# Optimization experiments

Measured on AMD Instinct MI355X. Metric: run time of the kernel, lower is better.

The kernel has to match this reference:

```python
import jax, jax.numpy as jnp
import numpy as np

B, S, D_IN, D_MODEL, H = 4, 2048, 1024, 1024, 16
DEPTH = D_MODEL // H  # 64


def setup_inputs() -> dict:
    key = jax.random.key(0)
    ks = jax.random.split(key, 8)
    scale = 1.0 / np.sqrt(D_IN)
    q = jax.random.normal(ks[0], (B, S, D_IN), dtype=jnp.float32)
    k = jax.random.normal(ks[1], (B, S, D_IN), dtype=jnp.float32)
    v = jax.random.normal(ks[2], (B, S, D_IN), dtype=jnp.float32)
    # causal additive mask: 1.0 where attention is disallowed (strictly upper triangle)
    mask = jnp.triu(jnp.ones((S, S), dtype=jnp.float32), k=1)[None, None]
    # parameters stored as [in, out] so projection is x @ W
    wq = jax.random.normal(ks[3], (D_IN, D_MODEL), dtype=jnp.float32) * scale
    wk = jax.random.normal(ks[4], (D_IN, D_MODEL), dtype=jnp.float32) * scale
    wv = jax.random.normal(ks[5], (D_IN, D_MODEL), dtype=jnp.float32) * scale
    wd = jax.random.normal(ks[6], (D_MODEL, D_MODEL), dtype=jnp.float32) * (1.0 / np.sqrt(D_MODEL))
    bd = jax.random.normal(ks[7], (D_MODEL,), dtype=jnp.float32) * 0.01
    return {"q": q, "k": k, "v": v, "mask": mask,
            "wq": wq, "wk": wk, "wv": wv, "wd": wd, "bd": bd}


def _split_heads(x):
    # [B, S, D_MODEL] -> [B, H, S, DEPTH]
    return x.reshape(B, S, H, DEPTH).transpose(0, 2, 1, 3)


def reference(q, k, v, mask, wq, wk, wv, wd, bd):
    qh = _split_heads(q @ wq)
    kh = _split_heads(k @ wk)
    vh = _split_heads(v @ wv)
    logits = jnp.einsum('bhqd,bhkd->bhqk', qh, kh) / np.sqrt(DEPTH)
    logits = logits + mask * (-1e9)
    attn = jax.nn.softmax(logits, axis=-1)  # [B, H, S, S]
    ctx = jnp.einsum('bhqk,bhkd->bhqd', attn, vh)
    concat = ctx.transpose(0, 2, 1, 3).reshape(B, S, D_MODEL)
    out = concat @ wd + bd
    return out, attn
```

## Files before the change

kernel.cpp:

```cpp
#include <hip/hip_runtime.h>
#include <hip/hip_bf16.h>
#include <math.h>

#define B_  4
#define S_  2048
#define DM  1024
#define H_  16

typedef __attribute__((ext_vector_type(8))) short short8;
typedef __attribute__((ext_vector_type(4))) short short4v;
typedef __attribute__((ext_vector_type(4))) float f32x4;

#define BAR_LGKM() do { \
    asm volatile("s_waitcnt lgkmcnt(0)" ::: "memory"); \
    __builtin_amdgcn_s_barrier(); \
    __builtin_amdgcn_sched_barrier(0); \
} while (0)

#define WAVE_FENCE() do { \
    asm volatile("s_waitcnt lgkmcnt(0)" ::: "memory"); \
    __builtin_amdgcn_sched_barrier(0); \
} while (0)

typedef __attribute__((address_space(3))) short      lds_s;
typedef __attribute__((address_space(1))) const short glb_s;
#define GLD16(g, l) __builtin_amdgcn_global_load_lds((glb_s*)(g), (lds_s*)(l), 16, 0, 0)

__device__ __forceinline__ short bf16b(float f) {
    __hip_bfloat16 h = __float2bfloat16(f);
    short s; __builtin_memcpy(&s, &h, 2);
    return s;
}

__device__ __forceinline__ float bf2f(short s) {
    unsigned int u = ((unsigned int)(unsigned short)s) << 16;
    float f; __builtin_memcpy(&f, &u, 4);
    return f;
}

__device__ __forceinline__ short8 cvt8(float4 a, float4 b) {
    short8 o;
    o[0] = bf16b(a.x); o[1] = bf16b(a.y); o[2] = bf16b(a.z); o[3] = bf16b(a.w);
    o[4] = bf16b(b.x); o[5] = bf16b(b.y); o[6] = bf16b(b.z); o[7] = bf16b(b.w);
    return o;
}

__device__ __forceinline__ short8 ldfrag(const short* __restrict__ lds, int row, int c) {
    return *reinterpret_cast<const short8*>(lds + (((row << 3) + (c ^ (row & 7))) << 3));
}

__global__ __launch_bounds__(256)
void tcast(const float* __restrict__ W, short* __restrict__ WT) {
    __shared__ float tile[64][65];
    const int n0 = blockIdx.x << 6, k0 = blockIdx.y << 6;
    const int t = threadIdx.x;
    #pragma unroll
    for (int i = 0; i < 16; ++i) {
        int f = i * 256 + t, r = f >> 6, c = f & 63;
        tile[r][c] = W[(size_t)(k0 + r) * DM + n0 + c];
    }
    __syncthreads();
    #pragma unroll
    for (int i = 0; i < 16; ++i) {
        int f = i * 256 + t, r = f >> 6, c = f & 63;
        WT[(size_t)(n0 + r) * DM + k0 + c] = bf16b(tile[c][r]);
    }
}

template<int EPI, int AF32>
__global__ __launch_bounds__(256)
void gemm_nt(const void* __restrict__ Av, const short* __restrict__ BT,
             const float* __restrict__ bias, short* __restrict__ Cb,
             float* __restrict__ Cf) {
    __shared__ __align__(16) short lA[128 * 64];
    __shared__ __align__(16) short lB[128 * 64];
    const int K = 1024;
    const short* A16 = (const short*)Av;
    const float* A32 = (const float*)Av;
    const int id = blockIdx.x;
    const int swz = ((id & 7) << 6) + (id >> 3);
    const int bm = swz >> 3, bn = swz & 7;
    const int t = threadIdx.x, w = t >> 6, l = t & 63, lg = l >> 4, lr = l & 15;
    const int wm = w >> 1, wn = w & 1;

    const int srow = t >> 1, sw = srow & 7, codd = t & 1;
    const size_t arow = (size_t)(bm * 128 + srow) * K;
    short* la = lA + (srow << 6);

    const int grow = l >> 3;
    const int gcol = ((l & 7) ^ grow) << 3;
    const short* Bg  = BT + (size_t)(bn * 128 + w * 32 + grow) * K + gcol;
    short*       lBw = lB + ((w * 32) << 6);
    const short* Ag  = A16 + (size_t)(bm * 128 + w * 32 + grow) * K + gcol;
    short*       lAw = lA + ((w * 32) << 6);

    f32x4 acc[4][4] = {};
    float4 fa[4][2];
    if (AF32) {
        #pragma unroll
        for (int j = 0; j < 4; ++j) {
            const float* p = A32 + arow + ((codd + (j << 1)) << 3);
            fa[j][0] = *reinterpret_cast<const float4*>(p);
            fa[j][1] = *reinterpret_cast<const float4*>(p + 4);
        }
    }

    for (int k0 = 0; k0 < K; k0 += 64) {
        __syncthreads();
        if (AF32) {
            #pragma unroll
            for (int j = 0; j < 4; ++j) {
                const int c = (codd + (j << 1)) ^ sw;
                *reinterpret_cast<short8*>(la + (c << 3)) = cvt8(fa[j][0], fa[j][1]);
            }
        } else {
            #pragma unroll
            for (int i = 0; i < 4; ++i)
                GLD16(Ag + k0 + (size_t)(i << 3) * K, lAw + (i << 9));
        }
        #pragma unroll
        for (int i = 0; i < 4; ++i)
            GLD16(Bg + k0 + (size_t)(i << 3) * K, lBw + (i << 9));
        __syncthreads();
        if (AF32 && k0 + 64 < K) {
            #pragma unroll
            for (int j = 0; j < 4; ++j) {
                const float* p = A32 + arow + k0 + 64 + ((codd + (j << 1)) << 3);
                fa[j][0] = *reinterpret_cast<const float4*>(p);
                fa[j][1] = *reinterpret_cast<const float4*>(p + 4);
            }
        }
        #pragma unroll
        for (int kk = 0; kk < 2; ++kk) {
            short8 af[4], bfr[4];
            #pragma unroll
            for (int fm = 0; fm < 4; ++fm) af[fm]  = ldfrag(lA, wm * 64 + fm * 16 + lr, kk * 4 + lg);
            #pragma unroll
            for (int fn = 0; fn < 4; ++fn) bfr[fn] = ldfrag(lB, wn * 64 + fn * 16 + lr, kk * 4 + lg);
            #pragma unroll
            for (int fm = 0; fm < 4; ++fm)
                #pragma unroll
                for (int fn = 0; fn < 4; ++fn)
                    acc[fm][fn] = __builtin_amdgcn_mfma_f32_16x16x32_bf16(af[fm], bfr[fn], acc[fm][fn], 0, 0, 0);
        }
    }

    const int rb = bm * 128 + wm * 64 + (lg << 2);
    const int cb = bn * 128 + wn * 64 + lr;
    #pragma unroll
    for (int fm = 0; fm < 4; ++fm) {
        #pragma unroll
        for (int fn = 0; fn < 4; ++fn) {
            const int col = cb + fn * 16;
            if (EPI == 2) {
                const float bv = bias[col];
                #pragma unroll
                for (int r = 0; r < 4; ++r) {
                    const int row = rb + fm * 16 + r;
                    Cf[(size_t)row * DM + col] = acc[fm][fn][r] + bv;
                }
            } else if (EPI == 0) {
                const int h = col >> 6, d = col & 63;
                #pragma unroll
                for (int r = 0; r < 4; ++r) {
                    const int row = rb + fm * 16 + r;
                    const int b = row >> 11, s = row & 2047;
                    Cb[(((size_t)(b * H_ + h) * S_ + s) << 6) + d] = bf16b(acc[fm][fn][r]);
                }
            } else {
                const int h = col >> 6, d = col & 63;
                const int row0 = rb + fm * 16;
                const int b = row0 >> 11, s = row0 & 2047;
                short4v pk;
                #pragma unroll
                for (int r = 0; r < 4; ++r) pk[r] = bf16b(acc[fm][fn][r]);
                *reinterpret_cast<short4v*>(Cb + (((size_t)(b * H_ + h) << 6) + d) * S_ + s) = pk;
            }
        }
    }
}

__global__ __launch_bounds__(512, 4)
void attn_mfma(const short* __restrict__ Qh, const short* __restrict__ Kh,
               const short* __restrict__ VhT, float* __restrict__ attn,
               short* __restrict__ ctxb) {
    __shared__ __align__(16) short smem[128 * 64 + 8 * 16 * 64];
    short* lQ = smem;
    short* lK = smem;
    short* lV = smem + 64 * 64;
    short* lP = smem + 128 * 64;

    const int t = threadIdx.x, w = t >> 6, l = t & 63, lg = l >> 4, lr = l & 15;
    const int n   = (int)blockIdx.x;
    const int xcd = n & 7, rest = n >> 3;
    const int j   = rest & 15, mh = rest >> 4;
    const int bh  = (mh << 3) | xcd;
    const int qt  = 15 - j;
    const int q0  = qt << 7;
    const int h   = bh & 15, b = bh >> 4;
    const float SC = 0.18033688f;

    const short* Qg = Qh  + (((size_t)bh * S_ + q0) << 6);
    const short* Kg = Kh  + ((size_t)bh * S_ << 6);
    const short* Vg = VhT + ((size_t)bh << 6) * S_;

    const int wrow = w * 16;
    const int rloc = q0 + wrow + (lg << 2);
    const int wlast = q0 + wrow + 15;
    const int Kw  = wlast >> 6;
    const int nkb = (q0 + 128) >> 6;

    {
        const int row = t >> 2, c0 = (t & 3) << 1, sw = row & 7;
        const short* src = Qg + ((size_t)row << 6) + (c0 << 3);
        short8 v0 = *reinterpret_cast<const short8*>(src);
        short8 v1 = *reinterpret_cast<const short8*>(src + 8);
        *reinterpret_cast<short8*>(lQ + (((row << 3) + ((c0    ) ^ sw)) << 3)) = v0;
        *reinterpret_cast<short8*>(lQ + (((row << 3) + ((c0 + 1) ^ sw)) << 3)) = v1;
    }
    __syncthreads();

    const short8 aq0 = ldfrag(lQ, wrow + lr, lg);
    const short8 aq1 = ldfrag(lQ, wrow + lr, lg + 4);

    const int srow = t >> 3, sc = t & 7;
    const int sslot = ((srow << 3) + (sc ^ (srow & 7))) << 3;
    const short* Kst = Kg + (srow << 6) + (sc << 3);
    const short* Vst = Vg + (size_t)srow * S_ + (sc << 3);

    float rsum[4] = {0.f, 0.f, 0.f, 0.f};
    short8 vk = *reinterpret_cast<const short8*>(Kst);
    for (int kb = 0; kb < nkb; ++kb) {
        BAR_LGKM();
        *reinterpret_cast<short8*>(lK + sslot) = vk;
        if (kb + 1 < nkb)
            vk = *reinterpret_cast<const short8*>(Kst + ((size_t)(kb + 1) << 12));
        BAR_LGKM();
        if (kb * 64 > wlast) continue;
        f32x4 acc[4] = {};
        #pragma unroll
        for (int t4 = 0; t4 < 4; ++t4) {
            short8 bk0 = ldfrag(lK, t4 * 16 + lr, lg);
            short8 bk1 = ldfrag(lK, t4 * 16 + lr, lg + 4);
            acc[t4] = __builtin_amdgcn_mfma_f32_16x16x32_bf16(aq0, bk0, acc[t4], 0, 0, 0);
            acc[t4] = __builtin_amdgcn_mfma_f32_16x16x32_bf16(aq1, bk1, acc[t4], 0, 0, 0);
        }
        if (kb * 64 + 63 <= q0 + wrow) {
            #pragma unroll
            for (int t4 = 0; t4 < 4; ++t4)
                #pragma unroll
                for (int r = 0; r < 4; ++r)
                    rsum[r] += exp2f(acc[t4][r] * SC);
        } else {
            #pragma unroll
            for (int t4 = 0; t4 < 4; ++t4) {
                const int cabs = kb * 64 + t4 * 16 + lr;
                #pragma unroll
                for (int r = 0; r < 4; ++r)
                    if (cabs <= rloc + r) rsum[r] += exp2f(acc[t4][r] * SC);
            }
        }
    }
    #pragma unroll
    for (int r = 0; r < 4; ++r) {
        #pragma unroll
        for (int m = 1; m < 16; m <<= 1) rsum[r] += __shfl_xor(rsum[r], m);
        rsum[r] = 1.f / rsum[r];
    }

    f32x4 ctxa[4] = {};
    short* lPw = lP + (w << 10);
    short8 vv;
    vk = *reinterpret_cast<const short8*>(Kst);
    vv = *reinterpret_cast<const short8*>(Vst);
    for (int kb = 0; kb < nkb; ++kb) {
        BAR_LGKM();
        *reinterpret_cast<short8*>(lK + sslot) = vk;
        *reinterpret_cast<short8*>(lV + sslot) = vv;
        if (kb + 1 < nkb) {
            vk = *reinterpret_cast<const short8*>(Kst + ((size_t)(kb + 1) << 12));
            vv = *reinterpret_cast<const short8*>(Vst + ((kb + 1) << 6));
        }
        BAR_LGKM();
        if (kb * 64 > wlast) continue;
        f32x4 acc[4] = {};
        #pragma unroll
        for (int t4 = 0; t4 < 4; ++t4) {
            short8 bk0 = ldfrag(lK, t4 * 16 + lr, lg);
            short8 bk1 = ldfrag(lK, t4 * 16 + lr, lg + 4);
            acc[t4] = __builtin_amdgcn_mfma_f32_16x16x32_bf16(aq0, bk0, acc[t4], 0, 0, 0);
            acc[t4] = __builtin_amdgcn_mfma_f32_16x16x32_bf16(aq1, bk1, acc[t4], 0, 0, 0);
        }
        const bool fullt = (kb * 64 + 63 <= q0 + wrow);
        #pragma unroll
        for (int t4 = 0; t4 < 4; ++t4) {
            const int cl = t4 * 16 + lr;
            const int cabs = kb * 64 + cl;
            #pragma unroll
            for (int r = 0; r < 4; ++r) {
                float p;
                if (!fullt && cabs > rloc + r) p = 0.f;
                else p = exp2f(acc[t4][r] * SC) * rsum[r];
                const int prow = (lg << 2) + r;
                lPw[(prow << 6) + (((t4 * 2 + (lr >> 3)) ^ (prow & 7)) << 3) + (l & 7)] = bf16b(p);
            }
        }
        WAVE_FENCE();
        {
            float* abase = attn + ((size_t)bh * S_ + q0 + wrow) * S_ + kb * 64;
            const int colc = (l & 15) << 2;
            const int ch0  = (l & 15) >> 1;
            const int half = ((l & 15) & 1) << 2;
            #pragma unroll
            for (int rr = 0; rr < 4; ++rr) {
                const int row = (l >> 4) + (rr << 2);
                short4v p4 = *reinterpret_cast<const short4v*>(
                    lPw + (row << 6) + ((ch0 ^ (row & 7)) << 3) + half);
                f32x4 pv = {bf2f(p4[0]), bf2f(p4[1]), bf2f(p4[2]), bf2f(p4[3])};
                *reinterpret_cast<f32x4*>(abase + (size_t)row * S_ + colc) = pv;
            }
        }
        short8 pa0 = ldfrag(lPw, lr, lg);
        short8 pa1 = ldfrag(lPw, lr, lg + 4);
        #pragma unroll
        for (int td = 0; td < 4; ++td) {
            short8 v0 = ldfrag(lV, td * 16 + lr, lg);
            short8 v1 = ldfrag(lV, td * 16 + lr, lg + 4);
            ctxa[td] = __builtin_amdgcn_mfma_f32_16x16x32_bf16(pa0, v0, ctxa[td], 0, 0, 0);
            ctxa[td] = __builtin_amdgcn_mfma_f32_16x16x32_bf16(pa1, v1, ctxa[td], 0, 0, 0);
        }
    }

    short* cbase = ctxb + ((size_t)(b * S_) + q0 + wrow + (lg << 2)) * DM + (h << 6);
    #pragma unroll
    for (int td = 0; td < 4; ++td)
        #pragma unroll
        for (int r = 0; r < 4; ++r)
            cbase[(size_t)r * DM + td * 16 + lr] = bf16b(ctxa[td][r]);

    {
        const f32x4 z = {0.f, 0.f, 0.f, 0.f};
        const int zs = (Kw + 1) << 6;
        const int colc = (l & 15) << 2;
        #pragma unroll
        for (int rr = 0; rr < 4; ++rr) {
            const int row = q0 + wrow + (l >> 4) + (rr << 2);
            float* rowp = attn + ((size_t)bh * S_ + row) * S_;
            for (int c = zs + colc; c < S_; c += 64)
                *reinterpret_cast<f32x4*>(rowp + c) = z;
        }
    }
}

extern "C" void kernel_launch(void* const* d_in, const int* in_sizes, int n_in,
                              void* d_out, int out_size, void* d_ws, size_t ws_size,
                              hipStream_t stream) {
    const float* q  = (const float*)d_in[0];
    const float* k  = (const float*)d_in[1];
    const float* v  = (const float*)d_in[2];
    const float* wq = (const float*)d_in[4];
    const float* wk = (const float*)d_in[5];
    const float* wv = (const float*)d_in[6];
    const float* wd = (const float*)d_in[7];
    const float* bd = (const float*)d_in[8];

    float* out  = (float*)d_out;
    float* attn = (float*)d_out + (size_t)B_ * S_ * DM;

    char* wsc = (char*)d_ws;
    short* ctxb = (short*)wsc;
    short* wT0 = (short*)(wsc + ((size_t)16 << 20));
    short* wT1 = (short*)(wsc + ((size_t)18 << 20));
    short* wT2 = (short*)(wsc + ((size_t)20 << 20));
    short* wT3 = (short*)(wsc + ((size_t)22 << 20));
    short* Qh  = (short*)(wsc + ((size_t)24 << 20));
    short* Kh  = (short*)(wsc + ((size_t)40 << 20));
    short* VhT = (short*)(wsc + ((size_t)56 << 20));

    const dim3 b256(256);
    hipLaunchKernelGGL(tcast, dim3(16, 16), b256, 0, stream, wq, wT0);
    hipLaunchKernelGGL(tcast, dim3(16, 16), b256, 0, stream, wk, wT1);
    hipLaunchKernelGGL(tcast, dim3(16, 16), b256, 0, stream, wv, wT2);
    hipLaunchKernelGGL(tcast, dim3(16, 16), b256, 0, stream, wd, wT3);

    hipLaunchKernelGGL((gemm_nt<0, 1>), dim3(512), b256, 0, stream, q, wT0, nullptr, Qh,  nullptr);
    hipLaunchKernelGGL((gemm_nt<0, 1>), dim3(512), b256, 0, stream, k, wT1, nullptr, Kh,  nullptr);
    hipLaunchKernelGGL((gemm_nt<1, 1>), dim3(512), b256, 0, stream, v, wT2, nullptr, VhT, nullptr);

    hipLaunchKernelGGL(attn_mfma, dim3(1024), dim3(512), 0, stream,
                       Qh, Kh, VhT, attn, ctxb);

    hipLaunchKernelGGL((gemm_nt<2, 0>), dim3(512), b256, 0, stream, ctxb, wT3, bd, nullptr, out);
}
```

Baseline: 450.2 us.

## Shrink attention query tile to 64 rows with 256-thread blocks

Result: no change. 441.6 us (-1.9%).

```diff
diff --git a/kernel.cpp b/kernel.cpp
--- a/kernel.cpp
+++ b/kernel.cpp
@@ -180,23 +180,23 @@
     }
 }
 
-__global__ __launch_bounds__(512, 4)
+__global__ __launch_bounds__(256, 4)
 void attn_mfma(const short* __restrict__ Qh, const short* __restrict__ Kh,
                const short* __restrict__ VhT, float* __restrict__ attn,
                short* __restrict__ ctxb) {
-    __shared__ __align__(16) short smem[128 * 64 + 8 * 16 * 64];
+    __shared__ __align__(16) short smem[64 * 64 * 2 + 4 * 16 * 64];
     short* lQ = smem;
     short* lK = smem;
     short* lV = smem + 64 * 64;
-    short* lP = smem + 128 * 64;
+    short* lP = smem + 64 * 64 * 2;
 
     const int t = threadIdx.x, w = t >> 6, l = t & 63, lg = l >> 4, lr = l & 15;
     const int n   = (int)blockIdx.x;
     const int xcd = n & 7, rest = n >> 3;
-    const int j   = rest & 15, mh = rest >> 4;
+    const int j   = rest & 31, mh = rest >> 5;
     const int bh  = (mh << 3) | xcd;
-    const int qt  = 15 - j;
-    const int q0  = qt << 7;
+    const int qt  = 31 - j;
+    const int q0  = qt << 6;
     const int h   = bh & 15, b = bh >> 4;
     const float SC = 0.18033688f;
 
@@ -206,37 +206,38 @@
 
     const int wrow = w * 16;
     const int rloc = q0 + wrow + (lg << 2);
-    const int wlast = q0 + wrow + 15;
-    const int Kw  = wlast >> 6;
-    const int nkb = (q0 + 128) >> 6;
+    const int nkb = qt + 1;
+
+    const int srow = t >> 2, sc0 = (t & 3) << 1, ssw = srow & 7;
+    const int sslot0 = ((srow << 3) + ((sc0    ) ^ ssw)) << 3;
+    const int sslot1 = ((srow << 3) + ((sc0 + 1) ^ ssw)) << 3;
+    const short* Kst = Kg + (srow << 6) + (sc0 << 3);
+    const short* Vst = Vg + (size_t)srow * S_ + (sc0 << 3);
 
     {
-        const int row = t >> 2, c0 = (t & 3) << 1, sw = row & 7;
-        const short* src = Qg + ((size_t)row << 6) + (c0 << 3);
+        const short* src = Qg + (srow << 6) + (sc0 << 3);
         short8 v0 = *reinterpret_cast<const short8*>(src);
         short8 v1 = *reinterpret_cast<const short8*>(src + 8);
-        *reinterpret_cast<short8*>(lQ + (((row << 3) + ((c0    ) ^ sw)) << 3)) = v0;
-        *reinterpret_cast<short8*>(lQ + (((row << 3) + ((c0 + 1) ^ sw)) << 3)) = v1;
+        *reinterpret_cast<short8*>(lQ + sslot0) = v0;
+        *reinterpret_cast<short8*>(lQ + sslot1) = v1;
     }
     __syncthreads();
 
     const short8 aq0 = ldfrag(lQ, wrow + lr, lg);
     const short8 aq1 = ldfrag(lQ, wrow + lr, lg + 4);
 
-    const int srow = t >> 3, sc = t & 7;
-    const int sslot = ((srow << 3) + (sc ^ (srow & 7))) << 3;
-    const short* Kst = Kg + (srow << 6) + (sc << 3);
-    const short* Vst = Vg + (size_t)srow * S_ + (sc << 3);
-
     float rsum[4] = {0.f, 0.f, 0.f, 0.f};
-    short8 vk = *reinterpret_cast<const short8*>(Kst);
+    short8 vk0 = *reinterpret_cast<const short8*>(Kst);
+    short8 vk1 = *reinterpret_cast<const short8*>(Kst + 8);
     for (int kb = 0; kb < nkb; ++kb) {
         BAR_LGKM();
-        *reinterpret_cast<short8*>(lK + sslot) = vk;
-        if (kb + 1 < nkb)
-            vk = *reinterpret_cast<const short8*>(Kst + ((size_t)(kb + 1) << 12));
+        *reinterpret_cast<short8*>(lK + sslot0) = vk0;
+        *reinterpret_cast<short8*>(lK + sslot1) = vk1;
+        if (kb + 1 < nkb) {
+            vk0 = *reinterpret_cast<const short8*>(Kst + ((size_t)(kb + 1) << 12));
+            vk1 = *reinterpret_cast<const short8*>(Kst + ((size_t)(kb + 1) << 12) + 8);
+        }
         BAR_LGKM();
-        if (kb * 64 > wlast) continue;
         f32x4 acc[4] = {};
         #pragma unroll
         for (int t4 = 0; t4 < 4; ++t4) {
@@ -245,7 +246,7 @@
             acc[t4] = __builtin_amdgcn_mfma_f32_16x16x32_bf16(aq0, bk0, acc[t4], 0, 0, 0);
             acc[t4] = __builtin_amdgcn_mfma_f32_16x16x32_bf16(aq1, bk1, acc[t4], 0, 0, 0);
         }
-        if (kb * 64 + 63 <= q0 + wrow) {
+        if (kb < qt) {
             #pragma unroll
             for (int t4 = 0; t4 < 4; ++t4)
                 #pragma unroll
@@ -270,19 +271,26 @@
 
     f32x4 ctxa[4] = {};
     short* lPw = lP + (w << 10);
-    short8 vv;
-    vk = *reinterpret_cast<const short8*>(Kst);
-    vv = *reinterpret_cast<const short8*>(Vst);
+    short8 vv0, vv1;
+    vk0 = *reinterpret_cast<const short8*>(Kst);
+    vk1 = *reinterpret_cast<const short8*>(Kst + 8);
+    vv0 = *reinterpret_cast<const short8*>(Vst);
+    vv1 = *reinterpret_cast<const short8*>(Vst + 8);
     for (int kb = 0; kb < nkb; ++kb) {
         BAR_LGKM();
-        *reinterpret_cast<short8*>(lK + sslot) = vk;
-        *reinterpret_cast<short8*>(lV + sslot) = vv;
+        *reinterpret_cast<short8*>(lK + sslot0) = vk0;
+        *reinterpret_cast<short8*>(lK + sslot1) = vk1;
+        *reinterpret_cast<short8*>(lV + sslot0) = vv0;
+        *reinterpret_cast<short8*>(lV + sslot1) = vv1;
         if (kb + 1 < nkb) {
-            vk = *reinterpret_cast<const short8*>(Kst + ((size_t)(kb + 1) << 12));
-            vv = *reinterpret_cast<const short8*>(Vst + ((kb + 1) << 6));
+            const short* kn = Kst + ((size_t)(kb + 1) << 12);
+            const short* vn = Vst + ((kb + 1) << 6);
+            vk0 = *reinterpret_cast<const short8*>(kn);
+            vk1 = *reinterpret_cast<const short8*>(kn + 8);
+            vv0 = *reinterpret_cast<const short8*>(vn);
+            vv1 = *reinterpret_cast<const short8*>(vn + 8);
         }
         BAR_LGKM();
-        if (kb * 64 > wlast) continue;
         f32x4 acc[4] = {};
         #pragma unroll
         for (int t4 = 0; t4 < 4; ++t4) {
@@ -291,7 +299,7 @@
             acc[t4] = __builtin_amdgcn_mfma_f32_16x16x32_bf16(aq0, bk0, acc[t4], 0, 0, 0);
             acc[t4] = __builtin_amdgcn_mfma_f32_16x16x32_bf16(aq1, bk1, acc[t4], 0, 0, 0);
         }
-        const bool fullt = (kb * 64 + 63 <= q0 + wrow);
+        const bool diag = (kb == qt);
         #pragma unroll
         for (int t4 = 0; t4 < 4; ++t4) {
             const int cl = t4 * 16 + lr;
@@ -299,7 +307,7 @@
             #pragma unroll
             for (int r = 0; r < 4; ++r) {
                 float p;
-                if (!fullt && cabs > rloc + r) p = 0.f;
+                if (diag && cabs > rloc + r) p = 0.f;
                 else p = exp2f(acc[t4][r] * SC) * rsum[r];
                 const int prow = (lg << 2) + r;
                 lPw[(prow << 6) + (((t4 * 2 + (lr >> 3)) ^ (prow & 7)) << 3) + (l & 7)] = bf16b(p);
@@ -340,7 +348,7 @@
 
     {
         const f32x4 z = {0.f, 0.f, 0.f, 0.f};
-        const int zs = (Kw + 1) << 6;
+        const int zs = (qt + 1) << 6;
         const int colc = (l & 15) << 2;
         #pragma unroll
         for (int rr = 0; rr < 4; ++rr) {
@@ -387,7 +395,7 @@
     hipLaunchKernelGGL((gemm_nt<0, 1>), dim3(512), b256, 0, stream, k, wT1, nullptr, Kh,  nullptr);
     hipLaunchKernelGGL((gemm_nt<1, 1>), dim3(512), b256, 0, stream, v, wT2, nullptr, VhT, nullptr);
 
-    hipLaunchKernelGGL(attn_mfma, dim3(1024), dim3(512), 0, stream,
+    hipLaunchKernelGGL(attn_mfma, dim3(2048), b256, 0, stream,
                        Qh, Kh, VhT, attn, ctxb);
 
     hipLaunchKernelGGL((gemm_nt<2, 0>), dim3(512), b256, 0, stream, ctxb, wT3, bd, nullptr, out);
```
